# Kernel optimization log

Measured on AMD Instinct MI355X. Metric: run time of the kernel, lower is better.

Reference implementation:

```python
import jax, jax.numpy as jnp
import numpy as np

V, E, H, K, B, T = 50000, 256, 256, 9, 128, 512


def lstm_dir(x, lens, Wih, Whh, b):
    # x: [B,T,E] -> h outputs [B,T,H], packed-sequence semantics:
    # state frozen and outputs zeroed for t >= lens[b].
    Bs, Ts, _ = x.shape
    Hh = Whh.shape[1]
    xw = jnp.einsum('bte,ge->btg', x, Wih) + b  # [B,T,4H] precomputed input proj
    valid = jnp.arange(Ts)[None, :] < lens[:, None]  # [B,T]

    def step(carry, inp):
        h, c = carry
        xw_t, v = inp  # [B,4H], [B]
        gates = xw_t + h @ Whh.T
        i, f, g, o = jnp.split(gates, 4, axis=-1)  # torch gate order i,f,g,o
        i = jax.nn.sigmoid(i)
        f = jax.nn.sigmoid(f)
        g = jnp.tanh(g)
        o = jax.nn.sigmoid(o)
        c_new = f * c + i * g
        h_new = o * jnp.tanh(c_new)
        v = v[:, None]
        return (jnp.where(v, h_new, h), jnp.where(v, c_new, c)), h_new * v

    init = (jnp.zeros((Bs, Hh), x.dtype), jnp.zeros((Bs, Hh), x.dtype))
    _, ys = jax.lax.scan(step, init, (jnp.swapaxes(xw, 0, 1), valid.T))
    return jnp.swapaxes(ys, 0, 1)


def reverse_by_len(x, lens):
    # per-row reversal within valid length; padding stays zero
    Ts = x.shape[1]
    t = jnp.arange(Ts)
    idx = jnp.clip(lens[:, None] - 1 - t[None, :], 0, Ts - 1)
    m = t[None, :] < lens[:, None]
    return jnp.take_along_axis(x, idx[:, :, None], axis=1) * m[:, :, None]


def crf_llh(em, tags, lens, start, end, trans):
    # torchcrf forward with reduction='sum': sum_b (gold score - logZ)
    Bs, Ts, Kk = em.shape
    mask = jnp.arange(Ts)[None, :] < lens[:, None]
    em_t = jnp.take_along_axis(em, tags[..., None], axis=-1)[..., 0]  # [B,T]
    score = start[tags[:, 0]] + em_t[:, 0]
    tr = trans[tags[:, :-1], tags[:, 1:]]  # [B,T-1]
    score = score + jnp.sum((tr + em_t[:, 1:]) * mask[:, 1:], axis=1)
    last_tag = jnp.take_along_axis(tags, (lens - 1)[:, None], axis=1)[:, 0]
    score = score + end[last_tag]

    def step(alpha, inp):
        e_t, m_t = inp  # [B,K], [B]
        nxt = jax.nn.logsumexp(alpha[:, :, None] + trans[None, :, :], axis=1) + e_t
        return jnp.where(m_t[:, None], nxt, alpha), None

    alpha0 = start[None, :] + em[:, 0]  # [B,K]
    alpha, _ = jax.lax.scan(step, alpha0,
                            (jnp.swapaxes(em[:, 1:], 0, 1), mask[:, 1:].T))
    logZ = jax.nn.logsumexp(alpha + end[None, :], axis=1)
    return jnp.sum(score - logZ)


def setup_inputs() -> dict:
    key = jax.random.key(0)
    ks = jax.random.split(key, 16)
    sentences = jax.random.randint(ks[0], (B, T), 0, V)
    tags = jax.random.randint(ks[1], (B, T), 0, K)
    length_list = jax.random.randint(ks[2], (B,), 1, T + 1)  # >=1 so mask[:,0] all true
    s = float(1.0 / np.sqrt(H))
    u = lambda k, sh: jax.random.uniform(k, sh, jnp.float32, -s, s)
    emb = jax.random.normal(ks[3], (V, E), jnp.float32) * float(np.sqrt(2.0 / E))
    return dict(
        sentences=sentences, tags=tags, length_list=length_list,
        emb=emb,
        Wih_f=u(ks[4], (4 * H, E)), Whh_f=u(ks[5], (4 * H, H)), b_f=u(ks[6], (4 * H,)),
        Wih_b=u(ks[7], (4 * H, E)), Whh_b=u(ks[8], (4 * H, H)), b_b=u(ks[9], (4 * H,)),
        W_out=u(ks[10], (K, 2 * H)), b_out=u(ks[11], (K,)),
        start=jax.random.uniform(ks[12], (K,), jnp.float32, -0.1, 0.1),
        end=jax.random.uniform(ks[13], (K,), jnp.float32, -0.1, 0.1),
        trans=jax.random.uniform(ks[14], (K, K), jnp.float32, -0.1, 0.1),
    )


def reference(sentences, tags, length_list, emb, Wih_f, Whh_f, b_f,
              Wih_b, Whh_b, b_b, W_out, b_out, start, end, trans):
    x = emb[sentences]  # [B,T,E]
    h_f = lstm_dir(x, length_list, Wih_f, Whh_f, b_f)
    x_rev = reverse_by_len(x, length_list)
    h_b = reverse_by_len(lstm_dir(x_rev, length_list, Wih_b, Whh_b, b_b), length_list)
    hcat = jnp.concatenate([h_f, h_b], axis=-1)  # [B,T,2H]
    # Dropout is identity in eval mode
    em = jnp.einsum('bth,kh->btk', hcat, W_out) + b_out  # [B,T,K]
    return crf_llh(em, tags, length_list, start, end, trans)
```

## Files before the change

kernel.cpp:

```cpp
#include <hip/hip_runtime.h>
#include <hip/hip_bf16.h>

typedef short v8s __attribute__((ext_vector_type(8)));
typedef int   v8i __attribute__((ext_vector_type(8)));
typedef float v4f __attribute__((ext_vector_type(4)));
typedef float v2f __attribute__((ext_vector_type(2)));

#define T_ 512

template<int HI>
__device__ __forceinline__ v2f cvt2(unsigned int wsrc){
  return __builtin_amdgcn_cvt_pk_f32_fp8((int)wsrc, HI);
}
__device__ __forceinline__ v2f rcp2(v2f d){
  return (v2f){__builtin_amdgcn_rcpf(d.x), __builtin_amdgcn_rcpf(d.y)};
}
__device__ __forceinline__ v2f tanh2(v2f x){
  v2f x2 = x*x;
  v2f num = x*(x2 + 27.f);
  v2f den = x2*9.f + 27.f;
  v2f r = num * rcp2(den);
  return (v2f){__builtin_amdgcn_fmed3f(r.x,-1.f,1.f),
               __builtin_amdgcn_fmed3f(r.y,-1.f,1.f)};
}
__device__ __forceinline__ v2f sigm2(v2f x){
  v2f y = x*0.5f;
  v2f y2 = y*y;
  v2f num = y*(y2 + 27.f);
  v2f den = y2*9.f + 27.f;
  v2f r = num * rcp2(den);
  v2f rc = (v2f){__builtin_amdgcn_fmed3f(r.x,-1.f,1.f),
                 __builtin_amdgcn_fmed3f(r.y,-1.f,1.f)};
  return rc*0.5f + 0.5f;
}
__device__ __forceinline__ int pi_col(int p){
  return ((p>>5)<<5) + ((p&1)<<4) + ((p&31)>>1);
}
__device__ __forceinline__ v8i ld32(const void* p){
  uint4 lo = *(const uint4*)p;
  uint4 hi = *(const uint4*)((const char*)p + 16);
  v8i r;
  r[0]=(int)lo.x; r[1]=(int)lo.y; r[2]=(int)lo.z; r[3]=(int)lo.w;
  r[4]=(int)hi.x; r[5]=(int)hi.y; r[6]=(int)hi.z; r[7]=(int)hi.w;
  return r;
}
__device__ __forceinline__ unsigned f2fp4(float x){
  unsigned s = (x < 0.f) ? 8u : 0u;
  float a = fabsf(x);
  unsigned m;
  if      (a < 0.25f) m=0u; else if (a < 0.75f) m=1u;
  else if (a < 1.25f) m=2u; else if (a < 1.75f) m=3u;
  else if (a < 2.5f ) m=4u; else if (a < 3.5f ) m=5u;
  else if (a < 5.f  ) m=6u; else m=7u;
  return s|m;
}
__device__ __forceinline__ unsigned pk8(float a, float b, float c, float d){
  int w = __builtin_amdgcn_cvt_pk_fp8_f32(a, b, 0, 0);
  w     = __builtin_amdgcn_cvt_pk_fp8_f32(c, d, w, 1);
  return (unsigned)w;
}
__device__ __forceinline__ unsigned enc4(v2f h){
  v2f t = h*4.f;
  unsigned b = 0;
  #pragma unroll
  for (int s=0;s<2;++s){
    float v = s ? t.y : t.x;
    float ax = __builtin_amdgcn_fmed3f(fabsf(v), 0.f, 4.f);
    float gl = fmaf(ax, 2.f, 12582912.f);
    float gh = ax + 12582912.f;
    unsigned ql = __builtin_bit_cast(unsigned, gl) & 7u;
    unsigned qh = (__builtin_bit_cast(unsigned, gh) & 7u) + 2u;
    unsigned c  = (ax > 1.75f) ? qh : ql;
    unsigned sg = (__builtin_bit_cast(unsigned, v) >> 28) & 8u;
    b |= (c | sg) << (4*s);
  }
  return b;
}

__global__ __launch_bounds__(256) void prep_wih8_k(
    const float* __restrict__ Wa, const float* __restrict__ Wb,
    unsigned char* __restrict__ out)
{
  int idx = blockIdx.x*256 + threadIdx.x;
  int lane = idx & 63;
  int t2 = idx >> 6;
  int ntile = t2 & 127;
  int kt = t2 >> 7;
  int n = ntile*16 + (lane&15);
  const float* W = (n < 1024) ? (Wa + (size_t)n*256) : (Wb + (size_t)(n-1024)*256);
  int k0 = kt*128 + (lane>>4)*32;
  unsigned words[8];
  #pragma unroll
  for (int e=0;e<8;++e)
    words[e] = pk8(W[k0+e*4], W[k0+e*4+1], W[k0+e*4+2], W[k0+e*4+3]);
  unsigned char* d = out + (size_t)idx*32;
  *(uint4*)(d)      = make_uint4(words[0], words[1], words[2], words[3]);
  *(uint4*)(d + 16) = make_uint4(words[4], words[5], words[6], words[7]);
}

__global__ __launch_bounds__(256) void prep_whh4_k(
    const float* __restrict__ Wf, const float* __restrict__ Wb,
    unsigned char* __restrict__ out)
{
  int idx = blockIdx.x*256 + threadIdx.x;
  int lane = idx & 63;
  int t2 = idx >> 6;
  int ntile = t2 & 63;
  int kt = (t2>>6) & 1;
  int dir = t2 >> 7;
  const float* W = dir ? Wb : Wf;
  int n = ntile*16 + (lane&15);
  int kbase = kt*128 + (lane>>4)*32;
  const float* row = W + (size_t)n*256;
  unsigned words[4];
  #pragma unroll
  for (int d4=0;d4<4;++d4){
    unsigned acc = 0;
    #pragma unroll
    for (int j=0;j<8;++j){
      float v = row[pi_col(kbase + d4*8 + j)] * 64.f;
      acc |= f2fp4(v) << (4*j);
    }
    words[d4] = acc;
  }
  *(uint4*)(out + (size_t)idx*16) = make_uint4(words[0], words[1], words[2], words[3]);
}

__global__ __launch_bounds__(256) void xw_gemm_k(
    const int* __restrict__ sent, const float* __restrict__ emb,
    const unsigned char* __restrict__ wihg, const int* __restrict__ lens,
    const float* __restrict__ bfv, const float* __restrict__ bbv,
    unsigned char* __restrict__ xw)
{
  int mt = blockIdx.x;
  if (((mt&3)<<7) >= lens[mt>>2]) return;
  __shared__ unsigned char A[128][272];
  int tid = threadIdx.x;
  {
    int row = tid>>1, half = tid&1;
    int tok = sent[mt*128 + row];
    const float4* s = (const float4*)(emb + (size_t)tok*256 + half*128);
    unsigned char* drow = &A[row][half*128];
    #pragma unroll
    for (int c4=0; c4<8; ++c4){
      unsigned w0[4];
      #pragma unroll
      for (int u=0; u<4; ++u){
        float4 v = s[c4*4+u];
        w0[u] = pk8(v.x, v.y, v.z, v.w);
      }
      *(uint4*)(drow + c4*16) = make_uint4(w0[0], w0[1], w0[2], w0[3]);
    }
  }
  __syncthreads();
  int w = tid>>6, lane = tid&63, lr = lane&15, lq = lane>>4;
  #pragma unroll 1
  for (int i4=0; i4<4; ++i4){
    int dnv = w*4 + i4;
    int dn = dnv>>3, v = dnv&7;
    const float* bb = dn ? bbv : bfv;
    float bias[8];
    #pragma unroll
    for (int e=0;e<8;++e){
      int q = e>>1, s = e&1;
      bias[e] = bb[q*256 + v*32 + s*16 + lr];
    }
    #pragma unroll 1
    for (int mh=0; mh<2; ++mh){
      v4f acc[8][4];
      #pragma unroll
      for (int e=0;e<8;++e)
        #pragma unroll
        for (int mm=0;mm<4;++mm) acc[e][mm] = (v4f){0.f,0.f,0.f,0.f};
      #pragma unroll
      for (int kt=0;kt<2;++kt){
        v8i a0 = ld32(&A[mh*64 +  0 + lr][kt*128 + lq*32]);
        v8i a1 = ld32(&A[mh*64 + 16 + lr][kt*128 + lq*32]);
        v8i a2 = ld32(&A[mh*64 + 32 + lr][kt*128 + lq*32]);
        v8i a3 = ld32(&A[mh*64 + 48 + lr][kt*128 + lq*32]);
        #pragma unroll
        for (int e=0;e<8;++e){
          int q = e>>1, s = e&1;
          int ntile = dn*64 + q*16 + v*2 + s;
          v8i bfr = ld32(wihg + ((size_t)(kt*128 + ntile)*64 + lane)*32);
          acc[e][0] = __builtin_amdgcn_mfma_scale_f32_16x16x128_f8f6f4(
                        a0, bfr, acc[e][0], 0,0, 0,0x7f7f7f7f, 0,0x7f7f7f7f);
          acc[e][1] = __builtin_amdgcn_mfma_scale_f32_16x16x128_f8f6f4(
                        a1, bfr, acc[e][1], 0,0, 0,0x7f7f7f7f, 0,0x7f7f7f7f);
          acc[e][2] = __builtin_amdgcn_mfma_scale_f32_16x16x128_f8f6f4(
                        a2, bfr, acc[e][2], 0,0, 0,0x7f7f7f7f, 0,0x7f7f7f7f);
          acc[e][3] = __builtin_amdgcn_mfma_scale_f32_16x16x128_f8f6f4(
                        a3, bfr, acc[e][3], 0,0, 0,0x7f7f7f7f, 0,0x7f7f7f7f);
        }
      }
      #pragma unroll
      for (int mm=0;mm<4;++mm){
        #pragma unroll
        for (int j=0;j<4;++j){
          int row = mt*128 + mh*64 + mm*16 + lq*4 + j;
          unsigned lo = pk8(acc[0][mm][j]+bias[0], acc[1][mm][j]+bias[1],
                            acc[2][mm][j]+bias[2], acc[3][mm][j]+bias[3]);
          unsigned hi = pk8(acc[4][mm][j]+bias[4], acc[5][mm][j]+bias[5],
                            acc[6][mm][j]+bias[6], acc[7][mm][j]+bias[7]);
          *(uint2*)(xw + ((size_t)dn*65536 + row)*1024 + v*128 + lr*8)
              = make_uint2(lo, hi);
        }
      }
    }
  }
}

__global__ __launch_bounds__(512,1) void lstm_k(
    const unsigned char* __restrict__ xw,
    const unsigned char* __restrict__ whh4,
    const int* __restrict__ lens,
    unsigned char* __restrict__ hout)
{
  int bid = blockIdx.x, dir = bid>>5, grp = bid&31;
  int tid = threadIdx.x, w = tid>>6, lane = tid&63, lr = lane&15, lq = lane>>4;
  __shared__ unsigned char hbuf[2][16][136];
  __shared__ int tmax_s;
  for (int i=tid*4; i<2*16*136; i+=512*4) *(unsigned int*)(&((unsigned char*)hbuf)[i]) = 0u;
  if (tid==0){
    int mx=0;
    for (int i=0;i<4;++i){ int l = lens[grp*4+i]; mx = l>mx? l:mx; }
    tmax_s = mx;
  }
  v8i wreg[16];
  const unsigned char* wb = whh4 + (size_t)dir*131072;
  #pragma unroll
  for (int kt=0;kt<2;++kt){
    #pragma unroll
    for (int nt=0;nt<8;++nt){
      int ntile = (nt>>1)*16 + w*2 + (nt&1);
      uint4 t = *(const uint4*)(wb + ((size_t)(kt*64 + ntile)*64 + lane)*16);
      v8i r;
      r[0]=(int)t.x; r[1]=(int)t.y; r[2]=(int)t.z; r[3]=(int)t.w;
      r[4]=0; r[5]=0; r[6]=0; r[7]=0;
      wreg[kt*8+nt] = r;
    }
  }
  int seq = grp*4 + lq;
  int ln = lens[seq];
  v2f cc = (v2f){0.f, 0.f};
  const size_t dbase = (size_t)dir*65536;
  const unsigned char* xbase = xw + (dbase + (size_t)seq*T_)*1024 + w*128 + lr*8;
  unsigned char* hbase = hout + (dbase + (size_t)seq*T_)*256 + w*32 + lr*2;
  unsigned char* lw0 = &hbuf[1][lq*4][w*16 + lr];
  unsigned char* lw1 = &hbuf[0][lq*4][w*16 + lr];
  const unsigned char* lr0 = &hbuf[0][lr][lq*16];
  const unsigned char* lr1 = &hbuf[1][lr][lq*16];
  __syncthreads();
  int tmax = tmax_s;
  uint2 xv = *(const uint2*)(xbase + (size_t)(dir ? (ln-1) : 0)*1024);

  #define STEP_BODY(TE_EXPR, POS_EXPR)                                         \
    int cur = t&1;                                                             \
    int tn = (t+1<tmax)? t+1 : t;                                              \
    int te = (TE_EXPR);                                                        \
    uint2 xn = *(const uint2*)(xbase + ((size_t)te<<10));                      \
    const unsigned char* lrd = cur? lr1 : lr0;                                 \
    v2f xi = cvt2<0>(xv.x), xf = cvt2<1>(xv.x);                                \
    v2f xg = cvt2<0>(xv.y), xo = cvt2<1>(xv.y);                                \
    v4f acc[8];                                                                \
    _Pragma("unroll")                                                          \
    for (int nt=0;nt<8;++nt) asm("" : "=v"(acc[nt]));                          \
    acc[0][0] = xi.x; acc[1][0] = xi.y;                                        \
    acc[2][0] = xf.x; acc[3][0] = xf.y;                                        \
    acc[4][0] = xg.x; acc[5][0] = xg.y;                                        \
    acc[6][0] = xo.x; acc[7][0] = xo.y;                                        \
    _Pragma("unroll")                                                          \
    for (int kt=0;kt<2;++kt){                                                  \
      uint4 hh = *(const uint4*)(lrd + kt*64);                                 \
      v8i a;                                                                   \
      a[0]=(int)hh.x; a[1]=(int)hh.y; a[2]=(int)hh.z; a[3]=(int)hh.w;          \
      a[4]=0; a[5]=0; a[6]=0; a[7]=0;                                          \
      _Pragma("unroll")                                                        \
      for (int nt=0;nt<8;++nt)                                                 \
        acc[nt] = __builtin_amdgcn_mfma_scale_f32_16x16x128_f8f6f4(            \
                    a, wreg[kt*8+nt], acc[nt], 4, 4,                           \
                    0, 0x7D7D7D7D, 0, 0x79797979);                             \
    }                                                                          \
    int pos = (POS_EXPR);                                                      \
    v2f gi = (v2f){acc[0][0], acc[1][0]};                                      \
    v2f gf = (v2f){acc[2][0], acc[3][0]};                                      \
    v2f gg = (v2f){acc[4][0], acc[5][0]};                                      \
    v2f go = (v2f){acc[6][0], acc[7][0]};                                      \
    v2f iv = sigm2(gi), fv = sigm2(gf), gv = tanh2(gg), ov = sigm2(go);        \
    v2f cn = fv*cc + iv*gv;                                                    \
    v2f hn = ov*tanh2(cn);                                                     \
    cc = cn;                                                                   \
    int hp = __builtin_amdgcn_cvt_pk_fp8_f32(hn.x, hn.y, 0, 0);                \
    *(unsigned short*)(hbase + ((size_t)pos<<8)) = (unsigned short)(hp&0xffff);\
    *(cur? lw1 : lw0) = (unsigned char)enc4(hn);                               \
    xv = xn;                                                                   \
    asm volatile("s_waitcnt lgkmcnt(0)" ::: "memory");                         \
    __builtin_amdgcn_s_barrier();                                              \
    __builtin_amdgcn_sched_barrier(0);

  if (dir == 0){
    for (int t=0; t<tmax; ++t){
      STEP_BODY(tn, t)
    }
  } else {
    for (int t=0; t<tmax; ++t){
      STEP_BODY((tn<ln)? (ln-1-tn) : tn, (t<ln)? (ln-1-t) : t)
    }
  }
  #undef STEP_BODY
}

__global__ __launch_bounds__(256) void em_k(
    const unsigned char* __restrict__ hout,
    const float* __restrict__ Wout, const float* __restrict__ bout,
    const int* __restrict__ lens,
    float* __restrict__ em)
{
  __shared__ float Ws[9*512];
  for (int i=threadIdx.x;i<9*512;i+=256){
    int k = i>>9, p = i&511;
    int d = p>>8, pp = p&255;
    Ws[i] = Wout[k*512 + d*256 + pi_col(pp)];
  }
  __syncthreads();
  int wv = blockIdx.x*4 + (threadIdx.x>>6);
  int lane = threadIdx.x & 63;
  int g = lane>>4, r = lane&15;
  int m = wv*4 + g;
  const unsigned char* hf = hout + (size_t)m*256 + r*16;
  const unsigned char* hb = hout + ((size_t)65536 + m)*256 + r*16;
  uint4 vf = *(const uint4*)hf;
  uint4 vb = *(const uint4*)hb;
  float xf[16], xb[16];
  {
    v2f d0=cvt2<0>(vf.x), d1=cvt2<1>(vf.x), d2=cvt2<0>(vf.y), d3=cvt2<1>(vf.y);
    v2f d4=cvt2<0>(vf.z), d5=cvt2<1>(vf.z), d6=cvt2<0>(vf.w), d7=cvt2<1>(vf.w);
    xf[0]=d0.x; xf[1]=d0.y; xf[2]=d1.x; xf[3]=d1.y;
    xf[4]=d2.x; xf[5]=d2.y; xf[6]=d3.x; xf[7]=d3.y;
    xf[8]=d4.x; xf[9]=d4.y; xf[10]=d5.x; xf[11]=d5.y;
    xf[12]=d6.x; xf[13]=d6.y; xf[14]=d7.x; xf[15]=d7.y;
  }
  {
    v2f d0=cvt2<0>(vb.x), d1=cvt2<1>(vb.x), d2=cvt2<0>(vb.y), d3=cvt2<1>(vb.y);
    v2f d4=cvt2<0>(vb.z), d5=cvt2<1>(vb.z), d6=cvt2<0>(vb.w), d7=cvt2<1>(vb.w);
    xb[0]=d0.x; xb[1]=d0.y; xb[2]=d1.x; xb[3]=d1.y;
    xb[4]=d2.x; xb[5]=d2.y; xb[6]=d3.x; xb[7]=d3.y;
    xb[8]=d4.x; xb[9]=d4.y; xb[10]=d5.x; xb[11]=d5.y;
    xb[12]=d6.x; xb[13]=d6.y; xb[14]=d7.x; xb[15]=d7.y;
  }
  float a[9];
  #pragma unroll
  for (int k=0;k<9;++k){
    float s = 0.f;
    #pragma unroll
    for (int e=0;e<16;++e)
      s += xf[e]*Ws[k*512 + r*16 + e] + xb[e]*Ws[k*512 + 256 + r*16 + e];
    a[k]=s;
  }
  #pragma unroll
  for (int k=0;k<9;++k){
    #pragma unroll
    for (int off=8; off; off>>=1) a[k] += __shfl_xor(a[k], off, 64);
  }
  int b = m>>9, t = m&511;
  if (r==0 && t < lens[b]){
    float* d = em + (size_t)m*9;
    #pragma unroll
    for (int k=0;k<9;++k) d[k] = a[k] + bout[k];
  }
}

__global__ __launch_bounds__(256) void crf_k(
    const float* __restrict__ em, const int* __restrict__ tags,
    const int* __restrict__ lens, const float* __restrict__ startv,
    const float* __restrict__ endv, const float* __restrict__ trans,
    float* __restrict__ out)
{
  int wid = blockIdx.x*4 + (threadIdx.x>>6);
  int lane = threadIdx.x & 63;
  const float* e = em + (size_t)wid*T_*9;
  const int* tg = tags + (size_t)wid*T_;
  int L = lens[wid];
  float p = 0.f;
  for (int t = 1+lane; t < L; t += 64)
    p += trans[tg[t-1]*9 + tg[t]] + e[(size_t)t*9 + tg[t]];
  if (lane==0) p += startv[tg[0]] + e[tg[0]] + endv[tg[L-1]];
  #pragma unroll
  for (int off=32; off; off>>=1) p += __shfl_xor(p, off, 64);
  float tcol[9];
  #pragma unroll
  for (int i=0;i<9;++i) tcol[i] = (lane<9) ? trans[i*9 + lane] : 0.f;
  float alpha = (lane<9) ? (startv[lane] + e[lane]) : -1e30f;
  for (int t=1; t<L; ++t){
    float vs[9]; float mx = -1e30f;
    #pragma unroll
    for (int i=0;i<9;++i){
      float ai = __shfl(alpha, i, 64);
      vs[i] = ai + tcol[i];
      mx = fmaxf(mx, vs[i]);
    }
    float s = 0.f;
    #pragma unroll
    for (int i=0;i<9;++i) s += __expf(vs[i]-mx);
    float na = mx + __logf(s) + ((lane<9)? e[(size_t)t*9+lane] : 0.f);
    alpha = (lane<9) ? na : -1e30f;
  }
  float v = (lane<9) ? (alpha + endv[lane]) : -1e30f;
  float mx = v;
  #pragma unroll
  for (int off=32; off; off>>=1) mx = fmaxf(mx, __shfl_xor(mx, off, 64));
  float s = __expf(v-mx);
  #pragma unroll
  for (int off=32; off; off>>=1) s += __shfl_xor(s, off, 64);
  float logZ = mx + __logf(s);
  if (lane==0) atomicAdd(out, p - logZ);
}

extern "C" void kernel_launch(void* const* d_in, const int* in_sizes, int n_in,
                              void* d_out, int out_size, void* d_ws, size_t ws_size,
                              hipStream_t stream)
{
  const int*   sent  = (const int*)d_in[0];
  const int*   tags  = (const int*)d_in[1];
  const int*   lens  = (const int*)d_in[2];
  const float* emb   = (const float*)d_in[3];
  const float* Wih_f = (const float*)d_in[4];
  const float* Whh_f = (const float*)d_in[5];
  const float* b_f   = (const float*)d_in[6];
  const float* Wih_b = (const float*)d_in[7];
  const float* Whh_b = (const float*)d_in[8];
  const float* b_b   = (const float*)d_in[9];
  const float* Wout  = (const float*)d_in[10];
  const float* bout  = (const float*)d_in[11];
  const float* startv= (const float*)d_in[12];
  const float* endv  = (const float*)d_in[13];
  const float* trans = (const float*)d_in[14];
  char* ws = (char*)d_ws;
  unsigned char* wihg8 = (unsigned char*)(ws);
  unsigned char* whh4  = (unsigned char*)(ws + (size_t)524288);
  unsigned char* xw    = (unsigned char*)(ws + (size_t)1048576);
  unsigned char* hout  = (unsigned char*)(ws + (size_t)135266304);
  float* em            = (float*)(ws + (size_t)168820736);
  float* outp = (float*)d_out;

  (void)hipMemsetAsync(outp, 0, sizeof(float), stream);
  prep_wih8_k<<<64, 256, 0, stream>>>(Wih_f, Wih_b, wihg8);
  prep_whh4_k<<<64, 256, 0, stream>>>(Whh_f, Whh_b, whh4);
  xw_gemm_k<<<512, 256, 0, stream>>>(sent, emb, wihg8, lens, b_f, b_b, xw);
  lstm_k<<<64, 512, 0, stream>>>(xw, whh4, lens, hout);
  em_k<<<4096, 256, 0, stream>>>(hout, Wout, bout, lens, em);
  crf_k<<<32, 256, 0, stream>>>(em, tags, lens, startv, endv, trans, outp);
}
```

Baseline: 704.5 us.

## Stage recurrent LSTM weights in LDS instead of holding them in registers

The recurrent weight tiles for each direction (128 KB) are copied into shared memory once at kernel start. Each timestep then reads its 16 B operand per MFMA from LDS instead of keeping 16 weight fragments resident in VGPRs. This frees a large block of registers and drops the zero-fill of the upper operand lanes. In exchange it adds 16 LDS reads per step to the serial recurrence's critical path. The hidden-state LDS write is also moved ahead of the global output store so the value needed by the next step is issued first.

```diff
diff --git a/kernel.cpp b/kernel.cpp
--- a/kernel.cpp
+++ b/kernel.cpp
@@ -218,27 +218,20 @@
 {
   int bid = blockIdx.x, dir = bid>>5, grp = bid&31;
   int tid = threadIdx.x, w = tid>>6, lane = tid&63, lr = lane&15, lq = lane>>4;
+  __shared__ unsigned char wlds[131072];
   __shared__ unsigned char hbuf[2][16][136];
   __shared__ int tmax_s;
+  {
+    const unsigned char* wsrc = whh4 + (size_t)dir*131072;
+    #pragma unroll 4
+    for (int i = tid*16; i < 131072; i += 512*16)
+      *(uint4*)(wlds + i) = *(const uint4*)(wsrc + i);
+  }
   for (int i=tid*4; i<2*16*136; i+=512*4) *(unsigned int*)(&((unsigned char*)hbuf)[i]) = 0u;
   if (tid==0){
     int mx=0;
     for (int i=0;i<4;++i){ int l = lens[grp*4+i]; mx = l>mx? l:mx; }
     tmax_s = mx;
-  }
-  v8i wreg[16];
-  const unsigned char* wb = whh4 + (size_t)dir*131072;
-  #pragma unroll
-  for (int kt=0;kt<2;++kt){
-    #pragma unroll
-    for (int nt=0;nt<8;++nt){
-      int ntile = (nt>>1)*16 + w*2 + (nt&1);
-      uint4 t = *(const uint4*)(wb + ((size_t)(kt*64 + ntile)*64 + lane)*16);
-      v8i r;
-      r[0]=(int)t.x; r[1]=(int)t.y; r[2]=(int)t.z; r[3]=(int)t.w;
-      r[4]=0; r[5]=0; r[6]=0; r[7]=0;
-      wreg[kt*8+nt] = r;
-    }
   }
   int seq = grp*4 + lq;
   int ln = lens[seq];
@@ -250,6 +243,7 @@
   unsigned char* lw1 = &hbuf[0][lq*4][w*16 + lr];
   const unsigned char* lr0 = &hbuf[0][lr][lq*16];
   const unsigned char* lr1 = &hbuf[1][lr][lq*16];
+  const unsigned char* wbp = wlds + w*2048 + lane*16;
   __syncthreads();
   int tmax = tmax_s;
   uint2 xv = *(const uint2*)(xbase + (size_t)(dir ? (ln-1) : 0)*1024);
@@ -272,14 +266,18 @@
     _Pragma("unroll")                                                          \
     for (int kt=0;kt<2;++kt){                                                  \
       uint4 hh = *(const uint4*)(lrd + kt*64);                                 \
-      v8i a;                                                                   \
+      v8i a; asm("" : "=v"(a));                                                \
       a[0]=(int)hh.x; a[1]=(int)hh.y; a[2]=(int)hh.z; a[3]=(int)hh.w;          \
-      a[4]=0; a[5]=0; a[6]=0; a[7]=0;                                          \
+      const unsigned char* pk = wbp + kt*65536;                                \
       _Pragma("unroll")                                                        \
-      for (int nt=0;nt<8;++nt)                                                 \
+      for (int nt=0;nt<8;++nt){                                                \
+        uint4 tb = *(const uint4*)(pk + (nt>>1)*16384 + (nt&1)*1024);          \
+        v8i b; asm("" : "=v"(b));                                              \
+        b[0]=(int)tb.x; b[1]=(int)tb.y; b[2]=(int)tb.z; b[3]=(int)tb.w;        \
         acc[nt] = __builtin_amdgcn_mfma_scale_f32_16x16x128_f8f6f4(            \
-                    a, wreg[kt*8+nt], acc[nt], 4, 4,                           \
+                    a, b, acc[nt], 4, 4,                                       \
                     0, 0x7D7D7D7D, 0, 0x79797979);                             \
+      }                                                                        \
     }                                                                          \
     int pos = (POS_EXPR);                                                      \
     v2f gi = (v2f){acc[0][0], acc[1][0]};                                      \
@@ -290,9 +288,9 @@
     v2f cn = fv*cc + iv*gv;                                                    \
     v2f hn = ov*tanh2(cn);                                                     \
     cc = cn;                                                                   \
+    *(cur? lw1 : lw0) = (unsigned char)enc4(hn);                               \
     int hp = __builtin_amdgcn_cvt_pk_fp8_f32(hn.x, hn.y, 0, 0);                \
-    *(unsigned short*)(hbase + ((size_t)pos<<8)) = (unsigned short)(hp&0xffff);\
-    *(cur? lw1 : lw0) = (unsigned char)enc4(hn);                               \
+    *(unsigned short*)(hbase + ((size_t)pos<<8)) = (unsigned short)hp;         \
     xv = xn;                                                                   \
     asm volatile("s_waitcnt lgkmcnt(0)" ::: "memory");                         \
     __builtin_amdgcn_s_barrier();                                              \
```

After: 778.8 us. 1.11x slower.
